# Optimization experiments

Measured on AMD Instinct MI355X. Metric: run time of the kernel, lower is better.

Reference implementation:

```python
import jax, jax.numpy as jnp
import numpy as np

DIM_Q = 512
DIM_K = 512
DIM_V = 512
NUM_HEADS = 8
B, NQ, NK = 4, 2048, 2048


def _linear_init(key, d_in, d_out):
    kw, kb = jax.random.split(key)
    bound = 1.0 / np.sqrt(d_in)
    W = jax.random.uniform(kw, (d_in, d_out), minval=-bound, maxval=bound, dtype=jnp.float32)
    b = jax.random.uniform(kb, (d_out,), minval=-bound, maxval=bound, dtype=jnp.float32)
    return W, b


def setup_inputs() -> dict:
    key = jax.random.key(0)
    ks = jax.random.split(key, 6)
    Q = jax.random.normal(ks[0], (B, NQ, DIM_Q), dtype=jnp.float32)
    K = jax.random.normal(ks[1], (B, NK, DIM_K), dtype=jnp.float32)
    Wq, bq = _linear_init(ks[2], DIM_Q, DIM_V)
    Wk, bk = _linear_init(ks[3], DIM_K, DIM_V)
    Wv, bv = _linear_init(ks[4], DIM_K, DIM_V)
    Wo, bo = _linear_init(ks[5], DIM_V, DIM_V)
    ln0_g = jnp.ones((DIM_V,), jnp.float32)
    ln0_b = jnp.zeros((DIM_V,), jnp.float32)
    ln1_g = jnp.ones((DIM_V,), jnp.float32)
    ln1_b = jnp.zeros((DIM_V,), jnp.float32)
    return {"Q": Q, "K": K, "Wq": Wq, "bq": bq, "Wk": Wk, "bk": bk,
            "Wv": Wv, "bv": bv, "Wo": Wo, "bo": bo,
            "ln0_g": ln0_g, "ln0_b": ln0_b, "ln1_g": ln1_g, "ln1_b": ln1_b}


def _layer_norm(x, g, b, eps=1e-5):
    mu = jnp.mean(x, axis=-1, keepdims=True)
    var = jnp.mean(jnp.square(x - mu), axis=-1, keepdims=True)
    return (x - mu) * jax.lax.rsqrt(var + eps) * g + b


def reference(Q, K, Wq, bq, Wk, bk, Wv, bv, Wo, bo, ln0_g, ln0_b, ln1_g, ln1_b):
    h = NUM_HEADS
    dh = DIM_V // h
    q = Q @ Wq + bq                      # [B, NQ, DIM_V]
    k = K @ Wk + bk                      # [B, NK, DIM_V]
    v = K @ Wv + bv                      # [B, NK, DIM_V]
    qh = q.reshape(B, NQ, h, dh)
    kh = k.reshape(B, NK, h, dh)
    vh = v.reshape(B, NK, h, dh)
    # NOTE: faithful to original — scale by sqrt(dim_V), not sqrt(head_dim)
    scores = jnp.einsum('bqhd,bkhd->bhqk', qh, kh) / jnp.sqrt(jnp.float32(DIM_V))
    A = jax.nn.softmax(scores, axis=-1)  # [B, h, NQ, NK]
    o = jnp.einsum('bhqk,bkhd->bqhd', A, vh) + qh
    H = o.reshape(B, NQ, DIM_V)          # residual with projected Q
    H = _layer_norm(H, ln0_g, ln0_b)
    H = H + jax.nn.relu(H @ Wo + bo)
    H = _layer_norm(H, ln1_g, ln1_b)
    return H
```

## Files before the change

kernel.cpp:

```cpp
#include <hip/hip_runtime.h>

typedef float f32x4 __attribute__((ext_vector_type(4)));
typedef float f32x16 __attribute__((ext_vector_type(16)));
typedef __bf16 bf16x8 __attribute__((ext_vector_type(8)));
typedef unsigned short u16;
typedef unsigned int u32;
typedef u16 u16x8 __attribute__((ext_vector_type(8)));
typedef u16 u16x4 __attribute__((ext_vector_type(4)));
typedef u32 u32x4 __attribute__((ext_vector_type(4)));

#define SCALE2F (0.044194173824159216f * 1.4426950408889634f)
#define UNSCALE (1.0f / SCALE2F)

__device__ __forceinline__ u16 f2bf(float x){ return __builtin_bit_cast(u16, (__bf16)x); }
__device__ __forceinline__ float bf2f(u16 h){ unsigned u = ((unsigned)h) << 16; return __builtin_bit_cast(float, u); }
__device__ __forceinline__ int swz(int r, int byteInRow){ return (r*128 + byteInRow) ^ ((r & 7) << 4); }
__device__ __forceinline__ void gload16(const void* g, void* l) {
  __builtin_amdgcn_global_load_lds(
      (const __attribute__((address_space(1))) void*)g,
      (__attribute__((address_space(3))) void*)l, 16, 0, 0);
}
__device__ __forceinline__ u32 cvtpk(float lo, float hi_) {
  u32 r;
  asm("v_cvt_pk_bf16_f32 %0, %1, %2" : "=v"(r) : "v"(lo), "v"(hi_));
  return r;
}
__device__ __forceinline__ void swap32(u32 &a, u32 &b) {
  asm("v_permlane32_swap_b32 %0, %1" : "+v"(a), "+v"(b));
}

#define MFMA(a,b,c)   __builtin_amdgcn_mfma_f32_16x16x32_bf16((a),(b),(c),0,0,0)
#define MFMA32(a,b,c) __builtin_amdgcn_mfma_f32_32x32x16_bf16((a),(b),(c),0,0,0)

__global__ __launch_bounds__(256) void wprep_k(
    const float* __restrict__ W0, const float* __restrict__ W1,
    const float* __restrict__ W2, const float* __restrict__ W3,
    u16* __restrict__ wt)
{
  __shared__ float tile[64][68];
  const float* Ws[4] = {W0, W1, W2, W3};
  const float* W = Ws[blockIdx.z];
  const float sc = (blockIdx.z == 0) ? SCALE2F : 1.0f;
  u16* out = wt + (size_t)blockIdx.z * 512 * 512;
  int k0 = blockIdx.x * 64, n0 = blockIdx.y * 64;
  int t = threadIdx.x;
  #pragma unroll
  for (int i = 0; i < 2; ++i) {
    int c = t + i*256; int r = c >> 3, k8 = c & 7;
    const float* src = W + (size_t)(k0 + r)*512 + n0 + k8*8;
    *(f32x4*)&tile[r][k8*8]     = *(const f32x4*)src;
    *(f32x4*)&tile[r][k8*8 + 4] = *(const f32x4*)(src + 4);
  }
  __syncthreads();
  #pragma unroll
  for (int i = 0; i < 2; ++i) {
    int c = t + i*256; int r = c >> 3, k8 = c & 7;
    u16x8 h;
    #pragma unroll
    for (int j = 0; j < 8; ++j) h[j] = f2bf(tile[k8*8 + j][r] * sc);
    *(u16x8*)(out + (size_t)(n0 + r)*512 + k0 + k8*8) = h;
  }
}

__global__ __launch_bounds__(512) void proj3_k(
    const float* __restrict__ Qin, const float* __restrict__ Kin,
    const u16* __restrict__ wt,
    const float* __restrict__ bq, const float* __restrict__ bk, const float* __restrict__ bv,
    u16* __restrict__ qbuf, u16* __restrict__ kbuf, u16* __restrict__ vt)
{
  __shared__ __align__(16) u16 lA[2][64*64];
  __shared__ __align__(16) u16 lB[2][128*64];
  int z = blockIdx.z;
  const float* A    = (z == 0) ? Qin : Kin;
  const u16*   Bt   = wt + (size_t)z * 262144;
  const float* bias = (z == 0) ? bq : (z == 1) ? bk : bv;
  const float bscale = (z == 0) ? SCALE2F : 1.0f;
  int row0 = blockIdx.x * 64, col0 = blockIdx.y * 128;
  int t = threadIdx.x, lane = t & 63, wid = t >> 6;
  int wr = wid >> 2, wc = wid & 3;
  int l15 = lane & 15, lg = lane >> 4;
  int ar = t >> 3, ak8 = t & 7;
  int br = t >> 3;
  int bsrc = (((t & 7) << 4) ^ ((br & 7) << 4)) >> 1;
  const float* Arow = A + (size_t)row0 * 512;
  const u16*   Brow = Bt + (size_t)col0 * 512;

  f32x4 acc[2][2] = {};

  #pragma unroll
  for (int i = 0; i < 2; ++i)
    gload16(Brow + (size_t)(br + i*64)*512 + bsrc, (char*)lB[0] + i*8192 + t*16);
  {
    const float* src = Arow + (size_t)ar*512 + ak8*8;
    f32x4 x0 = *(const f32x4*)src;
    f32x4 x1 = *(const f32x4*)(src + 4);
    u16x8 h;
    #pragma unroll
    for (int j = 0; j < 4; ++j) { h[j] = f2bf(x0[j]); h[j+4] = f2bf(x1[j]); }
    *(u16x8*)((char*)lA[0] + swz(ar, ak8*16)) = h;
  }
  __syncthreads();

  int cur = 0;
  for (int k0 = 0; k0 < 512; k0 += 64) {
    bool pf = (k0 + 64 < 512);
    f32x4 px0, px1;
    if (pf) {
      #pragma unroll
      for (int i = 0; i < 2; ++i)
        gload16(Brow + (size_t)(br + i*64)*512 + k0 + 64 + bsrc, (char*)lB[cur^1] + i*8192 + t*16);
      const float* src = Arow + (size_t)ar*512 + k0 + 64 + ak8*8;
      px0 = *(const f32x4*)src;
      px1 = *(const f32x4*)(src + 4);
    }
    const char* lAc = (const char*)lA[cur];
    const char* lBc = (const char*)lB[cur];
    #pragma unroll
    for (int ks = 0; ks < 2; ++ks) {
      bf16x8 af[2], bfv[2];
      #pragma unroll
      for (int m = 0; m < 2; ++m)
        af[m] = *(const bf16x8*)(lAc + swz(wr*32 + m*16 + l15, ks*64 + lg*16));
      #pragma unroll
      for (int n = 0; n < 2; ++n)
        bfv[n] = *(const bf16x8*)(lBc + swz(wc*32 + n*16 + l15, ks*64 + lg*16));
      #pragma unroll
      for (int m = 0; m < 2; ++m)
        #pragma unroll
        for (int n = 0; n < 2; ++n)
          acc[m][n] = MFMA(af[m], bfv[n], acc[m][n]);
    }
    if (pf) {
      u16x8 h;
      #pragma unroll
      for (int j = 0; j < 4; ++j) { h[j] = f2bf(px0[j]); h[j+4] = f2bf(px1[j]); }
      *(u16x8*)((char*)lA[cur^1] + swz(ar, ak8*16)) = h;
    }
    __syncthreads();
    cur ^= 1;
  }

  if (z < 2) {
    u16* out = z ? kbuf : qbuf;
    #pragma unroll
    for (int m = 0; m < 2; ++m) {
      int rowg = row0 + wr*32 + m*16 + lg*4;
      #pragma unroll
      for (int n = 0; n < 2; ++n) {
        int colg = col0 + wc*32 + n*16 + l15;
        float bvv = bias[colg] * bscale;
        #pragma unroll
        for (int r = 0; r < 4; ++r)
          out[(size_t)(rowg + r)*512 + colg] = f2bf(acc[m][n][r] + bvv);
      }
    }
  } else {
    #pragma unroll
    for (int m = 0; m < 2; ++m) {
      int rowg = row0 + wr*32 + m*16 + lg*4;
      int b = rowg >> 11, ntok = rowg & 2047;
      #pragma unroll
      for (int n = 0; n < 2; ++n) {
        int colg = col0 + wc*32 + n*16 + l15;
        float bvv = bias[colg];
        u16x4 hv;
        #pragma unroll
        for (int r = 0; r < 4; ++r) hv[r] = f2bf(acc[m][n][r] + bvv);
        *(u16x4*)(vt + ((size_t)b*512 + colg)*2048 + ntok) = hv;
      }
    }
  }
}

__global__ __launch_bounds__(512) void gemmo_k(
    const u16* __restrict__ A, const u16* __restrict__ Bt,
    const float* __restrict__ bias, u16* __restrict__ outb,
    const u16* __restrict__ resid)
{
  __shared__ __align__(16) u16 lA[2][64*64];
  __shared__ __align__(16) u16 lB[2][128*64];
  int row0 = blockIdx.x * 64, col0 = blockIdx.y * 128;
  int t = threadIdx.x, lane = t & 63, wid = t >> 6;
  int wr = wid >> 2, wc = wid & 3;
  int l15 = lane & 15, lg = lane >> 4;
  int ar = t >> 3;
  int asrc = (((t & 7) << 4) ^ ((ar & 7) << 4)) >> 1;
  const u16* Arow = A + (size_t)row0 * 512;
  const u16* Brow = Bt + (size_t)col0 * 512;
  f32x4 acc[2][2] = {};

  gload16(Arow + (size_t)ar*512 + asrc, (char*)lA[0] + t*16);
  #pragma unroll
  for (int i = 0; i < 2; ++i)
    gload16(Brow + (size_t)(ar + i*64)*512 + asrc, (char*)lB[0] + i*8192 + t*16);
  __syncthreads();

  int cur = 0;
  for (int k0 = 0; k0 < 512; k0 += 64) {
    if (k0 + 64 < 512) {
      gload16(Arow + (size_t)ar*512 + k0 + 64 + asrc, (char*)lA[cur^1] + t*16);
      #pragma unroll
      for (int i = 0; i < 2; ++i)
        gload16(Brow + (size_t)(ar + i*64)*512 + k0 + 64 + asrc, (char*)lB[cur^1] + i*8192 + t*16);
    }
    const char* lAc = (const char*)lA[cur];
    const char* lBc = (const char*)lB[cur];
    #pragma unroll
    for (int ks = 0; ks < 2; ++ks) {
      bf16x8 af[2], bfv[2];
      #pragma unroll
      for (int m = 0; m < 2; ++m)
        af[m] = *(const bf16x8*)(lAc + swz(wr*32 + m*16 + l15, ks*64 + lg*16));
      #pragma unroll
      for (int n = 0; n < 2; ++n)
        bfv[n] = *(const bf16x8*)(lBc + swz(wc*32 + n*16 + l15, ks*64 + lg*16));
      #pragma unroll
      for (int m = 0; m < 2; ++m)
        #pragma unroll
        for (int n = 0; n < 2; ++n)
          acc[m][n] = MFMA(af[m], bfv[n], acc[m][n]);
    }
    __syncthreads();
    cur ^= 1;
  }
  #pragma unroll
  for (int m = 0; m < 2; ++m) {
    int rowg = row0 + wr*32 + m*16 + lg*4;
    #pragma unroll
    for (int n = 0; n < 2; ++n) {
      int colg = col0 + wc*32 + n*16 + l15;
      float bvv = bias[colg];
      #pragma unroll
      for (int r = 0; r < 4; ++r) {
        size_t idx = (size_t)(rowg + r)*512 + colg;
        outb[idx] = f2bf(bf2f(resid[idx]) + fmaxf(acc[m][n][r] + bvv, 0.0f));
      }
    }
  }
}

__device__ __forceinline__ void mk_pb(const f32x16& s, float& ps, bf16x8& f0, bf16x8& f1) {
  float p[16];
  #pragma unroll
  for (int r = 0; r < 16; ++r) { p[r] = __builtin_amdgcn_exp2f(s[r]); ps += p[r]; }
  u32 a0 = cvtpk(p[0],  p[1]),  b0 = cvtpk(p[4],  p[5]);
  u32 a1 = cvtpk(p[2],  p[3]),  b1 = cvtpk(p[6],  p[7]);
  swap32(a0, b0); swap32(a1, b1);
  u32 a2 = cvtpk(p[8],  p[9]),  b2 = cvtpk(p[12], p[13]);
  u32 a3 = cvtpk(p[10], p[11]), b3 = cvtpk(p[14], p[15]);
  swap32(a2, b2); swap32(a3, b3);
  u32x4 w0 = {a0, a1, b0, b1};
  u32x4 w1 = {a2, a3, b2, b3};
  f0 = __builtin_bit_cast(bf16x8, w0);
  f1 = __builtin_bit_cast(bf16x8, w1);
}

__global__ __launch_bounds__(256, 2) void attn_k(
    const u16* __restrict__ qb, const u16* __restrict__ kb,
    const u16* __restrict__ vt, u16* __restrict__ opart, float* __restrict__ psb)
{
  __shared__ __align__(16) u16 lK[2][64*64];
  __shared__ __align__(16) u16 lV[2][64*64];

  int t = threadIdx.x, lane = t & 63, wid = t >> 6;
  int bh = blockIdx.y, b = bh >> 3, h = bh & 7;
  int zkv = blockIdx.z;
  int kvbeg = zkv * 1024;
  int q0 = blockIdx.x * 256 + wid * 64;
  int l31 = lane & 31, hi = lane >> 5;

  const u16* kbase = kb + ((size_t)b*2048)*512 + h*64;
  const u16* vbase = vt + ((size_t)b*512 + h*64)*2048;

  int sr = t >> 3;
  int ssrc = ((t & 7) ^ (sr & 7)) << 3;

#define STAGE(buf, kvoff)                                                              \
  gload16(kbase + (size_t)((kvoff) + sr)*512 + ssrc,       (char*)lK[buf] + t*16);     \
  gload16(kbase + (size_t)((kvoff) + 32 + sr)*512 + ssrc,  (char*)lK[buf] + 4096 + t*16); \
  gload16(vbase + (size_t)sr*2048 + (kvoff) + ssrc,        (char*)lV[buf] + t*16);     \
  gload16(vbase + (size_t)(32 + sr)*2048 + (kvoff) + ssrc, (char*)lV[buf] + 4096 + t*16);

  bf16x8 aqA[4], aqB[4];
  {
    const u16* qpA = qb + ((size_t)(b*2048 + q0 + l31))*512 + h*64 + hi*8;
    const u16* qpB = qpA + (size_t)32*512;
    #pragma unroll
    for (int ks = 0; ks < 4; ++ks) {
      aqA[ks] = *(const bf16x8*)(qpA + ks*16);
      aqB[ks] = *(const bf16x8*)(qpB + ks*16);
    }
  }

  f32x16 accA[2] = {}, accB[2] = {};
  float psA = 0.0f, psB = 0.0f;

  STAGE(0, kvbeg);
  __syncthreads();

  int cur = 0;
  for (int t0 = kvbeg; t0 < kvbeg + 1024; t0 += 64) {
    if (t0 + 64 < kvbeg + 1024) { STAGE(cur^1, t0 + 64); }
    const char* lKc = (const char*)lK[cur];
    const char* lVc = (const char*)lV[cur];
    bf16x8 pbA[4], pbB[4];
    #pragma unroll
    for (int n = 0; n < 2; ++n) {
      f32x16 s0 = {}, s1 = {};
      #pragma unroll
      for (int ks = 0; ks < 4; ++ks) {
        bf16x8 kf = *(const bf16x8*)(lKc + swz(n*32 + l31, ks*32 + hi*16));
        s0 = MFMA32(kf, aqA[ks], s0);
        s1 = MFMA32(kf, aqB[ks], s1);
      }
      mk_pb(s0, psA, pbA[2*n], pbA[2*n+1]);
      mk_pb(s1, psB, pbB[2*n], pbB[2*n+1]);
    }
    #pragma unroll
    for (int m = 0; m < 2; ++m)
      #pragma unroll
      for (int ks = 0; ks < 4; ++ks) {
        bf16x8 vf = *(const bf16x8*)(lVc + swz(m*32 + l31, ks*32 + hi*16));
        accA[m] = MFMA32(vf, pbA[ks], accA[m]);
        accB[m] = MFMA32(vf, pbB[ks], accB[m]);
      }
    __syncthreads();
    cur ^= 1;
  }
#undef STAGE
  psA += __shfl_xor(psA, 32, 64);
  psB += __shfl_xor(psB, 32, 64);
  u16* oA = opart + (((size_t)zkv*4 + b)*2048 + q0 + l31)*512 + h*64;
  u16* oB = oA + (size_t)32*512;
  #pragma unroll
  for (int m = 0; m < 2; ++m)
    #pragma unroll
    for (int rq = 0; rq < 4; ++rq) {
      u16x4 hA, hB;
      #pragma unroll
      for (int e = 0; e < 4; ++e) {
        hA[e] = f2bf(accA[m][rq*4 + e]);
        hB[e] = f2bf(accB[m][rq*4 + e]);
      }
      *(u16x4*)(oA + m*32 + rq*8 + hi*4) = hA;
      *(u16x4*)(oB + m*32 + rq*8 + hi*4) = hB;
    }
  if (hi == 0) {
    psb[((size_t)zkv*32 + bh)*2048 + q0 + l31]      = psA;
    psb[((size_t)zkv*32 + bh)*2048 + q0 + 32 + l31] = psB;
  }
}

__global__ __launch_bounds__(256) void ln0c_k(
    const u16* __restrict__ opart, const float* __restrict__ psb,
    const u16* __restrict__ qb, const float* __restrict__ gam,
    const float* __restrict__ bet, u16* __restrict__ yh)
{
  int t = threadIdx.x, lane = t & 63, w = t >> 6;
  size_t row = (size_t)blockIdx.x * 4 + w;
  int b = (int)(row >> 11), q = (int)(row & 2047);
  int head = lane >> 3;
  float sa = psb[((size_t)b*8 + head)*2048 + q] +
             psb[((size_t)32 + b*8 + head)*2048 + q];
  float inv = 1.0f / sa;
  const u16* xa = opart + row*512 + lane*8;
  const u16* xb = xa + (size_t)8192*512;
  u16x8 av  = *(const u16x8*)xa;
  u16x8 bv8 = *(const u16x8*)xb;
  u16x8 qr  = *(const u16x8*)(qb + row*512 + lane*8);
  float v[8];
  #pragma unroll
  for (int j = 0; j < 8; ++j)
    v[j] = (bf2f(av[j]) + bf2f(bv8[j]))*inv + bf2f(qr[j])*UNSCALE;
  float s = 0.0f, ss = 0.0f;
  #pragma unroll
  for (int j = 0; j < 8; ++j) { s += v[j]; ss += v[j]*v[j]; }
  #pragma unroll
  for (int m = 1; m < 64; m <<= 1) { s += __shfl_xor(s, m, 64); ss += __shfl_xor(ss, m, 64); }
  float mu = s * (1.0f/512.0f);
  float var = ss * (1.0f/512.0f) - mu*mu;
  float rs = rsqrtf(var + 1e-5f);
  const float* gp = gam + lane*8;
  const float* bp = bet + lane*8;
  f32x4 g0 = *(const f32x4*)gp, g1 = *(const f32x4*)(gp + 4);
  f32x4 be0 = *(const f32x4*)bp, be1 = *(const f32x4*)(bp + 4);
  u16x8 hv;
  #pragma unroll
  for (int j = 0; j < 4; ++j) {
    hv[j]   = f2bf((v[j]   - mu)*rs*g0[j] + be0[j]);
    hv[j+4] = f2bf((v[j+4] - mu)*rs*g1[j] + be1[j]);
  }
  *(u16x8*)(yh + row*512 + lane*8) = hv;
}

__global__ __launch_bounds__(256) void ln_k(
    const u16* __restrict__ x, const float* __restrict__ gam,
    const float* __restrict__ bet, float* __restrict__ y)
{
  int t = threadIdx.x, lane = t & 63, w = t >> 6;
  size_t row = (size_t)blockIdx.x * 4 + w;
  u16x8 xv = *(const u16x8*)(x + row*512 + lane*8);
  float v[8];
  #pragma unroll
  for (int j = 0; j < 8; ++j) v[j] = bf2f(xv[j]);
  float s = 0.0f, ss = 0.0f;
  #pragma unroll
  for (int j = 0; j < 8; ++j) { s += v[j]; ss += v[j]*v[j]; }
  #pragma unroll
  for (int m = 1; m < 64; m <<= 1) { s += __shfl_xor(s, m, 64); ss += __shfl_xor(ss, m, 64); }
  float mu = s * (1.0f/512.0f);
  float var = ss * (1.0f/512.0f) - mu*mu;
  float rs = rsqrtf(var + 1e-5f);
  const float* gp = gam + lane*8;
  const float* bp = bet + lane*8;
  f32x4 g0 = *(const f32x4*)gp, g1 = *(const f32x4*)(gp + 4);
  f32x4 b0 = *(const f32x4*)bp, b1 = *(const f32x4*)(bp + 4);
  f32x4 o0, o1;
  #pragma unroll
  for (int j = 0; j < 4; ++j) {
    o0[j] = (v[j]   - mu)*rs*g0[j] + b0[j];
    o1[j] = (v[j+4] - mu)*rs*g1[j] + b1[j];
  }
  float* yp = y + row*512 + lane*8;
  *(f32x4*)yp = o0;
  *(f32x4*)(yp + 4) = o1;
}

extern "C" void kernel_launch(void* const* d_in, const int* in_sizes, int n_in,
                              void* d_out, int out_size, void* d_ws, size_t ws_size,
                              hipStream_t stream)
{
  const float* Q   = (const float*)d_in[0];
  const float* K   = (const float*)d_in[1];
  const float* Wq  = (const float*)d_in[2];
  const float* bq  = (const float*)d_in[3];
  const float* Wk  = (const float*)d_in[4];
  const float* bk  = (const float*)d_in[5];
  const float* Wv  = (const float*)d_in[6];
  const float* bv  = (const float*)d_in[7];
  const float* Wo  = (const float*)d_in[8];
  const float* bo  = (const float*)d_in[9];
  const float* g0  = (const float*)d_in[10];
  const float* b0  = (const float*)d_in[11];
  const float* g1  = (const float*)d_in[12];
  const float* b1  = (const float*)d_in[13];

  char* ws = (char*)d_ws;
  u16*   wt    = (u16*)(ws + 0);
  u16*   qbuf  = (u16*)(ws + (2u<<20));
  u16*   kbuf  = (u16*)(ws + (10u<<20));
  u16*   vt    = (u16*)(ws + (18u<<20));
  u16*   opart = (u16*)(ws + (26u<<20));
  u16*   Gb    = (u16*)(ws + (44u<<20));
  float* psb   = (float*)(ws + (58u<<20));
  u16*   Hbuf  = (u16*)(ws + (10u<<20));

  wprep_k<<<dim3(8, 8, 4), 256, 0, stream>>>(Wq, Wk, Wv, Wo, wt);
  proj3_k<<<dim3(128, 4, 3), 512, 0, stream>>>(Q, K, wt, bq, bk, bv, qbuf, kbuf, vt);
  attn_k<<<dim3(8, 32, 2), 256, 0, stream>>>(qbuf, kbuf, vt, opart, psb);
  ln0c_k<<<2048, 256, 0, stream>>>(opart, psb, qbuf, g0, b0, Hbuf);
  gemmo_k<<<dim3(128, 4), 512, 0, stream>>>(Hbuf, wt + 3*262144, bo, Gb, Hbuf);
  ln_k<<<2048, 256, 0, stream>>>(Gb, g1, b1, (float*)d_out);
}
```

Measured before the change: 98.89 us.

## Triple-buffer K/V tiles in attention with partial vmcnt waits and MFMA priority

The attention kernel moves from double to triple buffering of K/V tiles in LDS and prefetches two tiles ahead. It replaces __syncthreads with explicit s_waitcnt vmcnt(4) plus s_barrier, so the loads for the next tile can stay in flight across iterations. It also raises wave priority around the MFMA sections with s_setprio. The cost is more LDS per block (48KB), and the Gb workspace buffer is moved to a new offset, which depends on the workspace being large enough.

```diff
diff --git a/kernel.cpp b/kernel.cpp
--- a/kernel.cpp
+++ b/kernel.cpp
@@ -259,8 +259,8 @@
     const u16* __restrict__ qb, const u16* __restrict__ kb,
     const u16* __restrict__ vt, u16* __restrict__ opart, float* __restrict__ psb)
 {
-  __shared__ __align__(16) u16 lK[2][64*64];
-  __shared__ __align__(16) u16 lV[2][64*64];
+  __shared__ __align__(16) u16 lK[3][64*64];
+  __shared__ __align__(16) u16 lV[3][64*64];
 
   int t = threadIdx.x, lane = t & 63, wid = t >> 6;
   int bh = blockIdx.y, b = bh >> 3, h = bh & 7;
@@ -268,6 +268,7 @@
   int kvbeg = zkv * 1024;
   int q0 = blockIdx.x * 256 + wid * 64;
   int l31 = lane & 31, hi = lane >> 5;
+  const int NT = 16;
 
   const u16* kbase = kb + ((size_t)b*2048)*512 + h*64;
   const u16* vbase = vt + ((size_t)b*512 + h*64)*2048;
@@ -296,26 +297,33 @@
   float psA = 0.0f, psB = 0.0f;
 
   STAGE(0, kvbeg);
-  __syncthreads();
-
-  int cur = 0;
-  for (int t0 = kvbeg; t0 < kvbeg + 1024; t0 += 64) {
-    if (t0 + 64 < kvbeg + 1024) { STAGE(cur^1, t0 + 64); }
-    const char* lKc = (const char*)lK[cur];
-    const char* lVc = (const char*)lV[cur];
+  STAGE(1, kvbeg + 64);
+  asm volatile("s_waitcnt vmcnt(4)" ::: "memory");
+  __builtin_amdgcn_s_barrier();
+  __builtin_amdgcn_sched_barrier(0);
+
+  int rd = 0, wr2 = 2;
+  for (int i = 0; i < NT; ++i) {
+    int t0 = kvbeg + i*64;
+    if (i + 2 < NT) { STAGE(wr2, t0 + 128); }
+    const char* lKc = (const char*)lK[rd];
+    const char* lVc = (const char*)lV[rd];
     bf16x8 pbA[4], pbB[4];
     #pragma unroll
     for (int n = 0; n < 2; ++n) {
       f32x16 s0 = {}, s1 = {};
+      __builtin_amdgcn_s_setprio(1);
       #pragma unroll
       for (int ks = 0; ks < 4; ++ks) {
         bf16x8 kf = *(const bf16x8*)(lKc + swz(n*32 + l31, ks*32 + hi*16));
         s0 = MFMA32(kf, aqA[ks], s0);
         s1 = MFMA32(kf, aqB[ks], s1);
       }
+      __builtin_amdgcn_s_setprio(0);
       mk_pb(s0, psA, pbA[2*n], pbA[2*n+1]);
       mk_pb(s1, psB, pbB[2*n], pbB[2*n+1]);
     }
+    __builtin_amdgcn_s_setprio(1);
     #pragma unroll
     for (int m = 0; m < 2; ++m)
       #pragma unroll
@@ -324,8 +332,15 @@
         accA[m] = MFMA32(vf, pbA[ks], accA[m]);
         accB[m] = MFMA32(vf, pbB[ks], accB[m]);
       }
-    __syncthreads();
-    cur ^= 1;
+    __builtin_amdgcn_s_setprio(0);
+    if (i + 1 < NT) {
+      if (i + 2 < NT) { asm volatile("s_waitcnt vmcnt(4)" ::: "memory"); }
+      else            { asm volatile("s_waitcnt vmcnt(0)" ::: "memory"); }
+      __builtin_amdgcn_s_barrier();
+      __builtin_amdgcn_sched_barrier(0);
+    }
+    rd  = (rd  == 2) ? 0 : rd + 1;
+    wr2 = (wr2 == 2) ? 0 : wr2 + 1;
   }
 #undef STAGE
   psA += __shfl_xor(psA, 32, 64);
@@ -451,8 +466,8 @@
   u16*   kbuf  = (u16*)(ws + (10u<<20));
   u16*   vt    = (u16*)(ws + (18u<<20));
   u16*   opart = (u16*)(ws + (26u<<20));
-  u16*   Gb    = (u16*)(ws + (44u<<20));
   float* psb   = (float*)(ws + (58u<<20));
+  u16*   Gb    = (u16*)(ws + (59u<<20));
   u16*   Hbuf  = (u16*)(ws + (10u<<20));
 
   wprep_k<<<dim3(8, 8, 4), 256, 0, stream>>>(Wq, Wk, Wv, Wo, wt);
```

New measurement: 101.0 us. 2.1% more time.

## Split attention work across eight waves with 32 query rows each

Applied to the files above, without the earlier changes.

The attention kernel now runs 512 threads per block, and each wave handles 32 query rows instead of 64. Each thread stages one K row chunk and one V row chunk instead of two of each, and the per-wave accumulator, score and Q-fragment register sets are halved. The goal is more waves to hide latency and a smaller register footprint. The cost is that each K/V fragment read from LDS now feeds one MFMA instead of two, so LDS reuse drops. The launch bound of 512 threads at 4 blocks may force register spills. The softmax row-sum becomes a tree reduction, and the Gb buffer is moved in the workspace.

```diff
diff --git a/kernel.cpp b/kernel.cpp
--- a/kernel.cpp
+++ b/kernel.cpp
@@ -242,7 +242,12 @@
 __device__ __forceinline__ void mk_pb(const f32x16& s, float& ps, bf16x8& f0, bf16x8& f1) {
   float p[16];
   #pragma unroll
-  for (int r = 0; r < 16; ++r) { p[r] = __builtin_amdgcn_exp2f(s[r]); ps += p[r]; }
+  for (int r = 0; r < 16; ++r) p[r] = __builtin_amdgcn_exp2f(s[r]);
+  float t0 = (p[0] + p[1])  + (p[2] + p[3]);
+  float t1 = (p[4] + p[5])  + (p[6] + p[7]);
+  float t2 = (p[8] + p[9])  + (p[10] + p[11]);
+  float t3 = (p[12] + p[13]) + (p[14] + p[15]);
+  ps += (t0 + t1) + (t2 + t3);
   u32 a0 = cvtpk(p[0],  p[1]),  b0 = cvtpk(p[4],  p[5]);
   u32 a1 = cvtpk(p[2],  p[3]),  b1 = cvtpk(p[6],  p[7]);
   swap32(a0, b0); swap32(a1, b1);
@@ -255,7 +260,7 @@
   f1 = __builtin_bit_cast(bf16x8, w1);
 }
 
-__global__ __launch_bounds__(256, 2) void attn_k(
+__global__ __launch_bounds__(512, 4) void attn_k(
     const u16* __restrict__ qb, const u16* __restrict__ kb,
     const u16* __restrict__ vt, u16* __restrict__ opart, float* __restrict__ psb)
 {
@@ -266,7 +271,7 @@
   int bh = blockIdx.y, b = bh >> 3, h = bh & 7;
   int zkv = blockIdx.z;
   int kvbeg = zkv * 1024;
-  int q0 = blockIdx.x * 256 + wid * 64;
+  int q0 = blockIdx.x * 256 + wid * 32;
   int l31 = lane & 31, hi = lane >> 5;
 
   const u16* kbase = kb + ((size_t)b*2048)*512 + h*64;
@@ -275,25 +280,19 @@
   int sr = t >> 3;
   int ssrc = ((t & 7) ^ (sr & 7)) << 3;
 
-#define STAGE(buf, kvoff)                                                              \
-  gload16(kbase + (size_t)((kvoff) + sr)*512 + ssrc,       (char*)lK[buf] + t*16);     \
-  gload16(kbase + (size_t)((kvoff) + 32 + sr)*512 + ssrc,  (char*)lK[buf] + 4096 + t*16); \
-  gload16(vbase + (size_t)sr*2048 + (kvoff) + ssrc,        (char*)lV[buf] + t*16);     \
-  gload16(vbase + (size_t)(32 + sr)*2048 + (kvoff) + ssrc, (char*)lV[buf] + 4096 + t*16);
-
-  bf16x8 aqA[4], aqB[4];
+#define STAGE(buf, kvoff)                                                        \
+  gload16(kbase + (size_t)((kvoff) + sr)*512 + ssrc, (char*)lK[buf] + t*16);     \
+  gload16(vbase + (size_t)sr*2048 + (kvoff) + ssrc,  (char*)lV[buf] + t*16);
+
+  bf16x8 aq[4];
   {
-    const u16* qpA = qb + ((size_t)(b*2048 + q0 + l31))*512 + h*64 + hi*8;
-    const u16* qpB = qpA + (size_t)32*512;
-    #pragma unroll
-    for (int ks = 0; ks < 4; ++ks) {
-      aqA[ks] = *(const bf16x8*)(qpA + ks*16);
-      aqB[ks] = *(const bf16x8*)(qpB + ks*16);
-    }
-  }
-
-  f32x16 accA[2] = {}, accB[2] = {};
-  float psA = 0.0f, psB = 0.0f;
+    const u16* qp = qb + ((size_t)(b*2048 + q0 + l31))*512 + h*64 + hi*8;
+    #pragma unroll
+    for (int ks = 0; ks < 4; ++ks) aq[ks] = *(const bf16x8*)(qp + ks*16);
+  }
+
+  f32x16 acc[2] = {};
+  float ps = 0.0f;
 
   STAGE(0, kvbeg);
   __syncthreads();
@@ -303,52 +302,41 @@
     if (t0 + 64 < kvbeg + 1024) { STAGE(cur^1, t0 + 64); }
     const char* lKc = (const char*)lK[cur];
     const char* lVc = (const char*)lV[cur];
-    bf16x8 pbA[4], pbB[4];
+    bf16x8 pb[4];
     #pragma unroll
     for (int n = 0; n < 2; ++n) {
-      f32x16 s0 = {}, s1 = {};
+      f32x16 s = {};
       #pragma unroll
       for (int ks = 0; ks < 4; ++ks) {
         bf16x8 kf = *(const bf16x8*)(lKc + swz(n*32 + l31, ks*32 + hi*16));
-        s0 = MFMA32(kf, aqA[ks], s0);
-        s1 = MFMA32(kf, aqB[ks], s1);
+        s = MFMA32(kf, aq[ks], s);
       }
-      mk_pb(s0, psA, pbA[2*n], pbA[2*n+1]);
-      mk_pb(s1, psB, pbB[2*n], pbB[2*n+1]);
+      mk_pb(s, ps, pb[2*n], pb[2*n+1]);
     }
     #pragma unroll
     for (int m = 0; m < 2; ++m)
       #pragma unroll
       for (int ks = 0; ks < 4; ++ks) {
         bf16x8 vf = *(const bf16x8*)(lVc + swz(m*32 + l31, ks*32 + hi*16));
-        accA[m] = MFMA32(vf, pbA[ks], accA[m]);
-        accB[m] = MFMA32(vf, pbB[ks], accB[m]);
+        acc[m] = MFMA32(vf, pb[ks], acc[m]);
       }
     __syncthreads();
     cur ^= 1;
   }
 #undef STAGE
-  psA += __shfl_xor(psA, 32, 64);
-  psB += __shfl_xor(psB, 32, 64);
+  ps += __shfl_xor(ps, 32, 64);
   u16* oA = opart + (((size_t)zkv*4 + b)*2048 + q0 + l31)*512 + h*64;
-  u16* oB = oA + (size_t)32*512;
   #pragma unroll
   for (int m = 0; m < 2; ++m)
     #pragma unroll
     for (int rq = 0; rq < 4; ++rq) {
-      u16x4 hA, hB;
-      #pragma unroll
-      for (int e = 0; e < 4; ++e) {
-        hA[e] = f2bf(accA[m][rq*4 + e]);
-        hB[e] = f2bf(accB[m][rq*4 + e]);
-      }
+      u16x4 hA;
+      #pragma unroll
+      for (int e = 0; e < 4; ++e) hA[e] = f2bf(acc[m][rq*4 + e]);
       *(u16x4*)(oA + m*32 + rq*8 + hi*4) = hA;
-      *(u16x4*)(oB + m*32 + rq*8 + hi*4) = hB;
-    }
-  if (hi == 0) {
-    psb[((size_t)zkv*32 + bh)*2048 + q0 + l31]      = psA;
-    psb[((size_t)zkv*32 + bh)*2048 + q0 + 32 + l31] = psB;
-  }
+    }
+  if (hi == 0)
+    psb[((size_t)zkv*32 + bh)*2048 + q0 + l31] = ps;
 }
 
 __global__ __launch_bounds__(256) void ln0c_k(
@@ -451,13 +439,13 @@
   u16*   kbuf  = (u16*)(ws + (10u<<20));
   u16*   vt    = (u16*)(ws + (18u<<20));
   u16*   opart = (u16*)(ws + (26u<<20));
-  u16*   Gb    = (u16*)(ws + (44u<<20));
   float* psb   = (float*)(ws + (58u<<20));
+  u16*   Gb    = (u16*)(ws + (59u<<20));
   u16*   Hbuf  = (u16*)(ws + (10u<<20));
 
   wprep_k<<<dim3(8, 8, 4), 256, 0, stream>>>(Wq, Wk, Wv, Wo, wt);
   proj3_k<<<dim3(128, 4, 3), 512, 0, stream>>>(Q, K, wt, bq, bk, bv, qbuf, kbuf, vt);
-  attn_k<<<dim3(8, 32, 2), 256, 0, stream>>>(qbuf, kbuf, vt, opart, psb);
+  attn_k<<<dim3(8, 32, 2), 512, 0, stream>>>(qbuf, kbuf, vt, opart, psb);
   ln0c_k<<<2048, 256, 0, stream>>>(opart, psb, qbuf, g0, b0, Hbuf);
   gemmo_k<<<dim3(128, 4), 512, 0, stream>>>(Hbuf, wt + 3*262144, bo, Gb, Hbuf);
   ln_k<<<2048, 256, 0, stream>>>(Gb, g1, b1, (float*)d_out);
```

After: 100.2 us. About the same (+1.4%).
